# Kernel tuning notes

Measured on AMD Instinct MI355X. Metric: run time of the kernel, lower is better.

Reference implementation:

```python
import jax, jax.numpy as jnp
import numpy as np

NUM_EXPERTS = 8
TOP_K = 2

def setup_inputs() -> dict:
    key = jax.random.key(0)
    ks = jax.random.split(key, 5)
    B, S, D, E, H = 4, 2048, 1024, NUM_EXPERTS, 4096
    scale = 0.02
    return {
        'x': jax.random.normal(ks[0], (B, S, D), dtype=jnp.float32),
        'router_w': jax.random.normal(ks[1], (D, E), dtype=jnp.float32) * scale,
        'router_b': jnp.zeros((E,), dtype=jnp.float32),
        'w1': jax.random.normal(ks[2], (E, D, H), dtype=jnp.float32) * scale,
        'b1': jnp.zeros((E, H), dtype=jnp.float32),
        'w2': jax.random.normal(ks[3], (E, H, D), dtype=jnp.float32) * scale,
        'b2': jnp.zeros((E, D), dtype=jnp.float32),
    }

def reference(x, router_w, router_b, w1, b1, w2, b2):
    B, S, D = x.shape
    E = router_b.shape[0]
    x_flat = x.reshape(-1, D)                       # [T, D], T = B*S
    logits = x_flat @ router_w + router_b          # [T, E]
    routing_weights = jax.nn.softmax(logits, axis=-1)
    # NOTE: original module computes & renormalizes top-k weights but never
    # applies them — outputs of selected experts are summed UNWEIGHTED.
    top_w, top_idx = jax.lax.top_k(routing_weights, TOP_K)  # [T, k]
    out_flat = jnp.zeros_like(x_flat)
    for e in range(E):  # fixed small expert count; dense compute + mask combine
        mask = jnp.any(top_idx == e, axis=-1)      # [T]
        h = jax.nn.gelu(x_flat @ w1[e] + b1[e], approximate=False)  # [T, H]
        y = h @ w2[e] + b2[e]                      # [T, D]
        out_flat = out_flat + jnp.where(mask[:, None], y, 0.0)
    return out_flat.reshape(B, S, D)
```

## Files before the change

### kernel.cpp

```cpp
#include <hip/hip_runtime.h>

#define T_TOKENS 8192
#define DIM 1024
#define NEXP 8
#define HID 4096
#define ROWS (2 * T_TOKENS)
#define ROWS_PAD (ROWS + 256)

#define META_COUNTS 0
#define META_OFFSET 16
#define META_TOP2   32
#define META_ROWPOS (32 + T_TOKENS)

typedef __attribute__((ext_vector_type(8))) short short8;
typedef __attribute__((ext_vector_type(4))) float f32x4;
typedef __attribute__((ext_vector_type(4))) unsigned short u16x4;

__device__ __forceinline__ unsigned short bf16bits(float f) {
  unsigned u = __builtin_bit_cast(unsigned, f);
  u += 0x7fffu + ((u >> 16) & 1u);
  return (unsigned short)(u >> 16);
}

__device__ __forceinline__ void gl_lds16(const void* g, void* l) {
  __builtin_amdgcn_global_load_lds(
      (const __attribute__((address_space(1))) unsigned int*)g,
      (__attribute__((address_space(3))) unsigned int*)l, 16, 0, 0);
}

__device__ __forceinline__ float gelu_tanh(float x) {
  float x3 = x * x * x;
  float z = 0.7978845608028654f * x + 0.035677408136300125f * x3;
  float az = fabsf(z);
  float e = exp2f(az * 2.885390081777927f);
  float t = 1.0f - 2.0f / (1.0f + e);
  t = copysignf(t, z);
  return 0.5f * x * (1.0f + t);
}

__global__ __launch_bounds__(256) void transpose_w_kernel(
    const float* __restrict__ in, unsigned short* __restrict__ out, int R, int C) {
  __shared__ float tile[64][65];
  const int e = blockIdx.z;
  const int r0 = blockIdx.y * 64, c0 = blockIdx.x * 64;
  const float* inp = in + (size_t)e * R * C;
  unsigned short* outp = out + (size_t)e * R * C;
  const int tr = threadIdx.x >> 4;
  const int tc = (threadIdx.x & 15) * 4;
#pragma unroll
  for (int s = 0; s < 64; s += 16) {
    f32x4 v = *(const f32x4*)(inp + (size_t)(r0 + tr + s) * C + c0 + tc);
    tile[tr + s][tc + 0] = v[0]; tile[tr + s][tc + 1] = v[1];
    tile[tr + s][tc + 2] = v[2]; tile[tr + s][tc + 3] = v[3];
  }
  __syncthreads();
#pragma unroll
  for (int s = 0; s < 64; s += 16) {
    int orow = c0 + tr + s;
    u16x4 u;
#pragma unroll
    for (int k = 0; k < 4; ++k) u[k] = bf16bits(tile[tc + k][tr + s]);
    *(u16x4*)(outp + (size_t)orow * R + r0 + tc) = u;
  }
}

__global__ __launch_bounds__(256) void router_kernel(
    const float* __restrict__ x, const float* __restrict__ rw,
    const float* __restrict__ rb, int* __restrict__ meta) {
  const int w = threadIdx.x >> 6;
  const int l = threadIdx.x & 63;
  const int t = blockIdx.x * 4 + w;
  const float* xr = x + (size_t)t * DIM + l * 16;
  double acc[8];
#pragma unroll
  for (int e = 0; e < 8; ++e) acc[e] = 0.0;
#pragma unroll
  for (int m = 0; m < 16; m += 4) {
    f32x4 xv = *(const f32x4*)(xr + m);
#pragma unroll
    for (int q = 0; q < 4; ++q) {
      double xs = (double)xv[q];
      const float* rwr = rw + (size_t)(l * 16 + m + q) * NEXP;
      f32x4 r0 = *(const f32x4*)rwr;
      f32x4 r1 = *(const f32x4*)(rwr + 4);
      acc[0] += xs * (double)r0[0]; acc[1] += xs * (double)r0[1];
      acc[2] += xs * (double)r0[2]; acc[3] += xs * (double)r0[3];
      acc[4] += xs * (double)r1[0]; acc[5] += xs * (double)r1[1];
      acc[6] += xs * (double)r1[2]; acc[7] += xs * (double)r1[3];
    }
  }
#pragma unroll
  for (int off = 32; off >= 1; off >>= 1) {
#pragma unroll
    for (int e = 0; e < 8; ++e) acc[e] += __shfl_down(acc[e], off);
  }
  if (l == 0) {
    double lg[8];
#pragma unroll
    for (int e = 0; e < 8; ++e) lg[e] = acc[e] + (double)rb[e];
    int e1 = 0; double b1v = lg[0];
#pragma unroll
    for (int e = 1; e < 8; ++e) if (lg[e] > b1v) { b1v = lg[e]; e1 = e; }
    int e2 = -1; double b2v = -1e300;
#pragma unroll
    for (int e = 0; e < 8; ++e) if (e != e1 && lg[e] > b2v) { b2v = lg[e]; e2 = e; }
    meta[META_TOP2 + t] = e1 | (e2 << 4);
  }
}

__global__ __launch_bounds__(1024) void assign_kernel(int* __restrict__ meta) {
  __shared__ int hist[NEXP][1024];
  __shared__ int own[NEXP][1024];
  const int tid = threadIdx.x;
#pragma unroll
  for (int e = 0; e < NEXP; ++e) { hist[e][tid] = 0; own[e][tid] = 0; }
  __syncthreads();
  int top2[8];
#pragma unroll
  for (int q = 0; q < 8; ++q) {
    int t = tid * 8 + q;
    int p = meta[META_TOP2 + t];
    top2[q] = p;
    hist[p & 15][tid] += 1;
    hist[(p >> 4) & 15][tid] += 1;
  }
#pragma unroll
  for (int e = 0; e < NEXP; ++e) own[e][tid] = hist[e][tid];
  __syncthreads();
  for (int off = 1; off < 1024; off <<= 1) {
    int add[NEXP];
#pragma unroll
    for (int e = 0; e < NEXP; ++e) add[e] = (tid >= off) ? hist[e][tid - off] : 0;
    __syncthreads();
#pragma unroll
    for (int e = 0; e < NEXP; ++e) hist[e][tid] += add[e];
    __syncthreads();
  }
  int offp[NEXP];
  {
    int o = 0;
#pragma unroll
    for (int e = 0; e < NEXP; ++e) { offp[e] = o; o += hist[e][1023]; }
  }
  if (tid == 0) {
#pragma unroll
    for (int e = 0; e < NEXP; ++e) {
      meta[META_COUNTS + e] = hist[e][1023];
      meta[META_OFFSET + e] = offp[e];
    }
  }
#pragma unroll
  for (int e = 0; e < NEXP; ++e) own[e][tid] = offp[e] + hist[e][tid] - own[e][tid];
#pragma unroll
  for (int q = 0; q < 8; ++q) {
    int t = tid * 8 + q;
    int p = top2[q];
    int e1 = p & 15, e2 = (p >> 4) & 15;
    int r1 = own[e1][tid]; own[e1][tid] = r1 + 1;
    int r2 = own[e2][tid]; own[e2][tid] = r2 + 1;
    meta[META_ROWPOS + 2 * t] = r1;
    meta[META_ROWPOS + 2 * t + 1] = r2;
  }
}

__global__ __launch_bounds__(256) void gather_kernel(
    const float* __restrict__ x, unsigned short* __restrict__ gx,
    const int* __restrict__ meta) {
  const int t = blockIdx.x;
  const int r1 = meta[META_ROWPOS + 2 * t];
  const int r2 = meta[META_ROWPOS + 2 * t + 1];
  const int i = threadIdx.x * 4;
  f32x4 v = *(const f32x4*)(x + (size_t)t * DIM + i);
  u16x4 u;
  u[0] = bf16bits(v[0]); u[1] = bf16bits(v[1]);
  u[2] = bf16bits(v[2]); u[3] = bf16bits(v[3]);
  *(u16x4*)(gx + (size_t)r1 * DIM + i) = u;
  *(u16x4*)(gx + (size_t)r2 * DIM + i) = u;
}

template <int ACT>
__global__ __launch_bounds__(256) void moe_gemm(
    const unsigned short* __restrict__ A, const unsigned short* __restrict__ Bt,
    const float* __restrict__ bias, void* __restrict__ C,
    const int* __restrict__ meta, int K, int N) {
  const int e = blockIdx.z;
  const int n_e = meta[META_COUNTS + e];
  const int mt = blockIdx.y;
  if (mt * 128 >= n_e) return;
  const int n0 = blockIdx.x * 128;
  const int row0 = meta[META_OFFSET + e] + mt * 128;
  const int mrem = n_e - mt * 128;

  __shared__ __align__(16) unsigned short As[128 * 64];
  __shared__ __align__(16) unsigned short Bs[128 * 64];

  const int tid = threadIdx.x;
  const int w = tid >> 6, l = tid & 63;
  const int wr = w >> 1, wc = w & 1;

  f32x4 acc[4][4] = {};

  const unsigned short* Bte = Bt + (size_t)e * N * K;

  for (int kt = 0; kt < K; kt += 64) {
#pragma unroll
    for (int it = 0; it < 4; ++it) {
      int idx = it * 2048 + tid * 8;
      int row = idx >> 6;
      int cp = (idx >> 3) & 7;
      int col = ((cp ^ (row & 7)) << 3);
      gl_lds16(A + (size_t)(row0 + row) * K + kt + col, &As[it * 2048 + w * 512]);
    }
#pragma unroll
    for (int it = 0; it < 4; ++it) {
      int idx = it * 2048 + tid * 8;
      int row = idx >> 6;
      int cp = (idx >> 3) & 7;
      int col = ((cp ^ (row & 7)) << 3);
      gl_lds16(Bte + (size_t)(n0 + row) * K + kt + col, &Bs[it * 2048 + w * 512]);
    }
    __syncthreads();
#pragma unroll
    for (int ks = 0; ks < 2; ++ks) {
      short8 av[4], bv[4];
#pragma unroll
      for (int i = 0; i < 4; ++i) {
        int r = wr * 64 + i * 16 + (l & 15);
        int c = ks * 4 + (l >> 4);
        av[i] = *(const short8*)&As[r * 64 + ((c ^ (r & 7)) << 3)];
      }
#pragma unroll
      for (int j = 0; j < 4; ++j) {
        int r = wc * 64 + j * 16 + (l & 15);
        int c = ks * 4 + (l >> 4);
        bv[j] = *(const short8*)&Bs[r * 64 + ((c ^ (r & 7)) << 3)];
      }
#pragma unroll
      for (int i = 0; i < 4; ++i)
#pragma unroll
        for (int j = 0; j < 4; ++j)
          acc[i][j] = __builtin_amdgcn_mfma_f32_16x16x32_bf16(av[i], bv[j], acc[i][j], 0, 0, 0);
    }
    __syncthreads();
  }

  const int lc = l & 15;
  const int lro = (l >> 4) << 2;
#pragma unroll
  for (int i = 0; i < 4; ++i) {
#pragma unroll
    for (int j = 0; j < 4; ++j) {
      int gn = n0 + wc * 64 + j * 16 + lc;
      float bz = bias[(size_t)e * N + gn];
#pragma unroll
      for (int r = 0; r < 4; ++r) {
        int lr = wr * 64 + i * 16 + lro + r;
        if (lr < mrem) {
          float v = acc[i][j][r] + bz;
          size_t off = (size_t)(row0 + lr) * N + gn;
          if (ACT == 1) {
            ((unsigned short*)C)[off] = bf16bits(gelu_tanh(v));
          } else {
            ((float*)C)[off] = v;
          }
        }
      }
    }
  }
}

__global__ __launch_bounds__(256) void combine_kernel(
    const float* __restrict__ y, const int* __restrict__ meta, float* __restrict__ out) {
  const int t = blockIdx.x;
  const int r1 = meta[META_ROWPOS + 2 * t];
  const int r2 = meta[META_ROWPOS + 2 * t + 1];
  const int i = threadIdx.x * 4;
  f32x4 a = *(const f32x4*)(y + (size_t)r1 * DIM + i);
  f32x4 b = *(const f32x4*)(y + (size_t)r2 * DIM + i);
  f32x4 o = a + b;
  *(f32x4*)(out + (size_t)t * DIM + i) = o;
}

extern "C" void kernel_launch(void* const* d_in, const int* in_sizes, int n_in,
                              void* d_out, int out_size, void* d_ws, size_t ws_size,
                              hipStream_t stream) {
  const float* x  = (const float*)d_in[0];
  const float* rw = (const float*)d_in[1];
  const float* rb = (const float*)d_in[2];
  const float* w1 = (const float*)d_in[3];
  const float* b1 = (const float*)d_in[4];
  const float* w2 = (const float*)d_in[5];
  const float* b2 = (const float*)d_in[6];
  float* out = (float*)d_out;

  char* p = (char*)d_ws;
  unsigned short* w1t = (unsigned short*)p; p += (size_t)NEXP * DIM * HID * 2;
  unsigned short* w2t = (unsigned short*)p; p += (size_t)NEXP * DIM * HID * 2;
  unsigned short* gx  = (unsigned short*)p; p += (size_t)ROWS_PAD * DIM * 2;
  unsigned short* h   = (unsigned short*)p; p += (size_t)ROWS_PAD * HID * 2;
  float*          y   = (float*)p;          p += (size_t)ROWS_PAD * DIM * 4;
  int*            meta = (int*)p;
  (void)in_sizes; (void)n_in; (void)out_size; (void)ws_size;

  transpose_w_kernel<<<dim3(HID / 64, DIM / 64, NEXP), 256, 0, stream>>>(w1, w1t, DIM, HID);
  transpose_w_kernel<<<dim3(DIM / 64, HID / 64, NEXP), 256, 0, stream>>>(w2, w2t, HID, DIM);

  router_kernel<<<T_TOKENS / 4, 256, 0, stream>>>(x, rw, rb, meta);
  assign_kernel<<<1, 1024, 0, stream>>>(meta);
  gather_kernel<<<T_TOKENS, 256, 0, stream>>>(x, gx, meta);

  moe_gemm<1><<<dim3(HID / 128, 64, NEXP), 256, 0, stream>>>(gx, w1t, b1, h, meta, DIM, HID);
  moe_gemm<0><<<dim3(DIM / 128, 64, NEXP), 256, 0, stream>>>(h, w2t, b2, y, meta, HID, DIM);

  combine_kernel<<<T_TOKENS, 256, 0, stream>>>(y, meta, out);
}
```

Measured before the change: 591.7 us.

## Split-K the second expert GEMM and store bf16 partials reduced in combine

The down-projection GEMM now splits its K=4096 reduction into two halves. The grid's y dimension is doubled so twice as many workgroups run, since that GEMM has only 8 N-tiles per expert and would otherwise leave the GPU underfilled. Each half writes its partial sum as bf16 to its own buffer, with the bias added only by the first half. The combine kernel then sums all four partials per token. This adds parallelism and halves the y write size, at the cost of bf16 rounding on the partial outputs and extra reads in combine.

Measured after the change: 593.7 us. No clear change (+0.3%).

```diff
diff --git a/kernel.cpp b/kernel.cpp
--- a/kernel.cpp
+++ b/kernel.cpp
@@ -20,6 +20,11 @@
   unsigned u = __builtin_bit_cast(unsigned, f);
   u += 0x7fffu + ((u >> 16) & 1u);
   return (unsigned short)(u >> 16);
+}
+
+__device__ __forceinline__ float bf2f(unsigned short s) {
+  unsigned u = (unsigned)s << 16;
+  return __builtin_bit_cast(float, u);
 }
 
 __device__ __forceinline__ void gl_lds16(const void* g, void* l) {
@@ -178,18 +183,21 @@
   *(u16x4*)(gx + (size_t)r2 * DIM + i) = u;
 }
 
-template <int ACT>
+template <int ACT, int KSPLIT>
 __global__ __launch_bounds__(256) void moe_gemm(
     const unsigned short* __restrict__ A, const unsigned short* __restrict__ Bt,
     const float* __restrict__ bias, void* __restrict__ C,
     const int* __restrict__ meta, int K, int N) {
   const int e = blockIdx.z;
   const int n_e = meta[META_COUNTS + e];
-  const int mt = blockIdx.y;
+  const int mt = (KSPLIT > 1) ? (blockIdx.y >> 1) : blockIdx.y;
+  const int kh = (KSPLIT > 1) ? (blockIdx.y & 1) : 0;
   if (mt * 128 >= n_e) return;
   const int n0 = blockIdx.x * 128;
   const int row0 = meta[META_OFFSET + e] + mt * 128;
   const int mrem = n_e - mt * 128;
+  const int kbeg = kh * (K / KSPLIT);
+  const int kend = kbeg + (K / KSPLIT);
 
   __shared__ __align__(16) unsigned short As[128 * 64];
   __shared__ __align__(16) unsigned short Bs[128 * 64];
@@ -202,7 +210,7 @@
 
   const unsigned short* Bte = Bt + (size_t)e * N * K;
 
-  for (int kt = 0; kt < K; kt += 64) {
+  for (int kt = kbeg; kt < kend; kt += 64) {
 #pragma unroll
     for (int it = 0; it < 4; ++it) {
       int idx = it * 2048 + tid * 8;
@@ -251,7 +259,7 @@
 #pragma unroll
     for (int j = 0; j < 4; ++j) {
       int gn = n0 + wc * 64 + j * 16 + lc;
-      float bz = bias[(size_t)e * N + gn];
+      float bz = (kh == 0) ? bias[(size_t)e * N + gn] : 0.0f;
 #pragma unroll
       for (int r = 0; r < 4; ++r) {
         int lr = wr * 64 + i * 16 + lro + r;
@@ -261,7 +269,7 @@
           if (ACT == 1) {
             ((unsigned short*)C)[off] = bf16bits(gelu_tanh(v));
           } else {
-            ((float*)C)[off] = v;
+            ((unsigned short*)C)[(size_t)kh * ROWS_PAD * DIM + off] = bf16bits(v);
           }
         }
       }
@@ -270,14 +278,21 @@
 }
 
 __global__ __launch_bounds__(256) void combine_kernel(
-    const float* __restrict__ y, const int* __restrict__ meta, float* __restrict__ out) {
+    const unsigned short* __restrict__ y, const int* __restrict__ meta,
+    float* __restrict__ out) {
   const int t = blockIdx.x;
   const int r1 = meta[META_ROWPOS + 2 * t];
   const int r2 = meta[META_ROWPOS + 2 * t + 1];
   const int i = threadIdx.x * 4;
-  f32x4 a = *(const f32x4*)(y + (size_t)r1 * DIM + i);
-  f32x4 b = *(const f32x4*)(y + (size_t)r2 * DIM + i);
-  f32x4 o = a + b;
+  const unsigned short* y1 = y + (size_t)ROWS_PAD * DIM;
+  u16x4 a0 = *(const u16x4*)(y  + (size_t)r1 * DIM + i);
+  u16x4 a1 = *(const u16x4*)(y1 + (size_t)r1 * DIM + i);
+  u16x4 b0 = *(const u16x4*)(y  + (size_t)r2 * DIM + i);
+  u16x4 b1 = *(const u16x4*)(y1 + (size_t)r2 * DIM + i);
+  f32x4 o;
+#pragma unroll
+  for (int k = 0; k < 4; ++k)
+    o[k] = (bf2f(a0[k]) + bf2f(a1[k])) + (bf2f(b0[k]) + bf2f(b1[k]));
   *(f32x4*)(out + (size_t)t * DIM + i) = o;
 }
 
@@ -298,7 +313,7 @@
   unsigned short* w2t = (unsigned short*)p; p += (size_t)NEXP * DIM * HID * 2;
   unsigned short* gx  = (unsigned short*)p; p += (size_t)ROWS_PAD * DIM * 2;
   unsigned short* h   = (unsigned short*)p; p += (size_t)ROWS_PAD * HID * 2;
-  float*          y   = (float*)p;          p += (size_t)ROWS_PAD * DIM * 4;
+  unsigned short* y   = (unsigned short*)p; p += (size_t)2 * ROWS_PAD * DIM * 2;
   int*            meta = (int*)p;
   (void)in_sizes; (void)n_in; (void)out_size; (void)ws_size;
 
@@ -309,8 +324,8 @@
   assign_kernel<<<1, 1024, 0, stream>>>(meta);
   gather_kernel<<<T_TOKENS, 256, 0, stream>>>(x, gx, meta);
 
-  moe_gemm<1><<<dim3(HID / 128, 64, NEXP), 256, 0, stream>>>(gx, w1t, b1, h, meta, DIM, HID);
-  moe_gemm<0><<<dim3(DIM / 128, 64, NEXP), 256, 0, stream>>>(h, w2t, b2, y, meta, HID, DIM);
+  moe_gemm<1, 1><<<dim3(HID / 128, 64, NEXP), 256, 0, stream>>>(gx, w1t, b1, h, meta, DIM, HID);
+  moe_gemm<0, 2><<<dim3(DIM / 128, 64 * 2, NEXP), 256, 0, stream>>>(h, w2t, b2, y, meta, HID, DIM);
 
   combine_kernel<<<T_TOKENS, 256, 0, stream>>>(y, meta, out);
 }
```

## Double-buffer LDS tiles in MoE GEMM to overlap global loads with MFMA

Applied to the files above, without the earlier changes.

Splits the A and B shared-memory tiles into two buffers. The next K-tile is issued via direct global-to-LDS loads while the current tile is read and fed to MFMAs, so there is one barrier per iteration instead of two. LDS fragment reads are hoisted ahead of the MFMA block and the wave priority is raised during the MFMA burst. The cost is double the LDS footprint, which may lower occupancy. Correctness relies on the manual vmcnt/lgkmcnt waits and barriers to order buffer reuse.

Result: slower. 749.7 us (+26.7%).

```diff
diff --git a/kernel.cpp b/kernel.cpp
--- a/kernel.cpp
+++ b/kernel.cpp
@@ -190,9 +190,10 @@
   const int n0 = blockIdx.x * 128;
   const int row0 = meta[META_OFFSET + e] + mt * 128;
   const int mrem = n_e - mt * 128;
-
-  __shared__ __align__(16) unsigned short As[128 * 64];
-  __shared__ __align__(16) unsigned short Bs[128 * 64];
+  const int NT = K >> 6;
+
+  __shared__ __align__(16) unsigned short As[2][128 * 64];
+  __shared__ __align__(16) unsigned short Bs[2][128 * 64];
 
   const int tid = threadIdx.x;
   const int w = tid >> 6, l = tid & 63;
@@ -200,16 +201,17 @@
 
   f32x4 acc[4][4] = {};
 
-  const unsigned short* Bte = Bt + (size_t)e * N * K;
-
-  for (int kt = 0; kt < K; kt += 64) {
+  const unsigned short* Ag = A + (size_t)row0 * K;
+  const unsigned short* Bg = Bt + (size_t)e * N * K + (size_t)n0 * K;
+
+  auto stage = [&](int buf, int kt) {
 #pragma unroll
     for (int it = 0; it < 4; ++it) {
       int idx = it * 2048 + tid * 8;
       int row = idx >> 6;
       int cp = (idx >> 3) & 7;
       int col = ((cp ^ (row & 7)) << 3);
-      gl_lds16(A + (size_t)(row0 + row) * K + kt + col, &As[it * 2048 + w * 512]);
+      gl_lds16(Ag + (size_t)row * K + kt + col, &As[buf][it * 2048 + w * 512]);
     }
 #pragma unroll
     for (int it = 0; it < 4; ++it) {
@@ -217,31 +219,48 @@
       int row = idx >> 6;
       int cp = (idx >> 3) & 7;
       int col = ((cp ^ (row & 7)) << 3);
-      gl_lds16(Bte + (size_t)(n0 + row) * K + kt + col, &Bs[it * 2048 + w * 512]);
-    }
-    __syncthreads();
+      gl_lds16(Bg + (size_t)row * K + kt + col, &Bs[buf][it * 2048 + w * 512]);
+    }
+  };
+
+  stage(0, 0);
+  asm volatile("s_waitcnt vmcnt(0)" ::: "memory");
+  __builtin_amdgcn_s_barrier();
+
+  int cur = 0;
+  for (int t = 0; t < NT; ++t) {
+    if (t + 1 < NT) stage(cur ^ 1, (t + 1) << 6);
+    const unsigned short* Ac = As[cur];
+    const unsigned short* Bc = Bs[cur];
+    short8 av[2][4], bv[2][4];
 #pragma unroll
     for (int ks = 0; ks < 2; ++ks) {
-      short8 av[4], bv[4];
+      const int c = ks * 4 + (l >> 4);
 #pragma unroll
       for (int i = 0; i < 4; ++i) {
         int r = wr * 64 + i * 16 + (l & 15);
-        int c = ks * 4 + (l >> 4);
-        av[i] = *(const short8*)&As[r * 64 + ((c ^ (r & 7)) << 3)];
+        av[ks][i] = *(const short8*)&Ac[r * 64 + ((c ^ (r & 7)) << 3)];
       }
 #pragma unroll
       for (int j = 0; j < 4; ++j) {
         int r = wc * 64 + j * 16 + (l & 15);
-        int c = ks * 4 + (l >> 4);
-        bv[j] = *(const short8*)&Bs[r * 64 + ((c ^ (r & 7)) << 3)];
+        bv[ks][j] = *(const short8*)&Bc[r * 64 + ((c ^ (r & 7)) << 3)];
       }
+    }
+    asm volatile("s_waitcnt lgkmcnt(0)" ::: "memory");
+    __builtin_amdgcn_sched_barrier(0);
+    __builtin_amdgcn_s_setprio(1);
+#pragma unroll
+    for (int ks = 0; ks < 2; ++ks)
 #pragma unroll
       for (int i = 0; i < 4; ++i)
 #pragma unroll
         for (int j = 0; j < 4; ++j)
-          acc[i][j] = __builtin_amdgcn_mfma_f32_16x16x32_bf16(av[i], bv[j], acc[i][j], 0, 0, 0);
-    }
-    __syncthreads();
+          acc[i][j] = __builtin_amdgcn_mfma_f32_16x16x32_bf16(av[ks][i], bv[ks][j], acc[i][j], 0, 0, 0);
+    __builtin_amdgcn_s_setprio(0);
+    asm volatile("s_waitcnt vmcnt(0)" ::: "memory");
+    __builtin_amdgcn_s_barrier();
+    cur ^= 1;
   }
 
   const int lc = l & 15;
```
